# Optimization experiments

Hardware: AMD Instinct MI355X
Metric: run time of the kernel (lower is better)

## Reference

```python
import jax, jax.numpy as jnp
import numpy as np

EMBED = 768
HEADS = 12
HEAD_DIM = EMBED // HEADS  # 64
NUM_CLS = 1
WIN = 16        # one-sided window radius
DIL = 4         # dilation
THETA = 10000.0
COORD_HIGH = 100000.0


def _rotate_half(x):
    # [..., x1, x2, ...] -> [..., -x2, x1, ...] over adjacent pairs
    x1 = x[..., 0::2]
    x2 = x[..., 1::2]
    return jnp.stack([-x2, x1], axis=-1).reshape(x.shape)


def _rope2d(x, coords):
    # x: (B, H, L, head_dim); coords: (B, L, 2) pixel coords
    half = HEAD_DIM // 2
    inv_freq = 1.0 / THETA ** (jnp.arange(0, half, 2, dtype=jnp.float32) / half)  # (half/2,)
    xy = coords.astype(jnp.float32) / COORD_HIGH
    fx = xy[..., 0:1] * inv_freq  # (B, L, half/2)
    fy = xy[..., 1:2] * inv_freq
    fx = jnp.repeat(fx, 2, axis=-1)  # (B, L, half)
    fy = jnp.repeat(fy, 2, axis=-1)
    freqs = jnp.concatenate([fx, fy], axis=-1)  # (B, L, head_dim)
    cos = jnp.cos(freqs)[:, None]  # (B, 1, L, head_dim)
    sin = jnp.sin(freqs)[:, None]
    return x * cos + _rotate_half(x) * sin


def setup_inputs() -> dict:
    key = jax.random.key(0)
    ks = jax.random.split(key, 5)
    B, L = 1, 4096
    S = L + NUM_CLS
    x = jax.random.normal(ks[0], (B, S, EMBED), jnp.float32)
    coords = jax.random.randint(ks[1], (B, L, 2), 0, 100000).astype(jnp.int32)
    qkv_w = jax.random.normal(ks[2], (3 * EMBED, EMBED), jnp.float32) * 0.02
    qkv_b = jnp.zeros((3 * EMBED,), jnp.float32)
    out_w = jax.random.normal(ks[3], (EMBED, EMBED), jnp.float32) * 0.02
    out_b = jnp.zeros((EMBED,), jnp.float32)
    return {"x": x, "coords": coords, "qkv_w": qkv_w, "qkv_b": qkv_b,
            "out_w": out_w, "out_b": out_b}


def reference(x, coords, qkv_w, qkv_b, out_w, out_b):
    B, S, E = x.shape
    L = S - NUM_CLS
    # QKV projection -> (3, B, H, S, hd)
    qkv = (x @ qkv_w.T + qkv_b).reshape(B, S, 3, HEADS, HEAD_DIM)
    qkv = qkv.transpose(2, 0, 3, 1, 4)
    q, k, v = qkv[0], qkv[1], qkv[2]
    # 2D RoPE on patch tokens only
    q = jnp.concatenate([q[:, :, :NUM_CLS], _rope2d(q[:, :, NUM_CLS:], coords)], axis=2)
    k = jnp.concatenate([k[:, :, :NUM_CLS], _rope2d(k[:, :, NUM_CLS:], coords)], axis=2)
    scale = 1.0 / np.sqrt(HEAD_DIM).astype(np.float32)

    q_cls, k_cls, v_cls = q[:, :, :NUM_CLS], k[:, :, :NUM_CLS], v[:, :, :NUM_CLS]
    q_p, k_p, v_p = q[:, :, NUM_CLS:], k[:, :, NUM_CLS:], v[:, :, NUM_CLS:]

    # CLS (global) queries attend to everything
    cls_scores = jnp.einsum('bhqd,bhkd->bhqk', q_cls, k) * scale
    cls_out = jnp.einsum('bhqk,bhkd->bhqd', jax.nn.softmax(cls_scores, axis=-1), v)

    # Patch queries: single softmax over [CLS keys | dilated local window]
    win_len = 2 * WIN + 1
    pos = jnp.arange(L)
    rel = (jnp.arange(win_len) - WIN) * DIL
    key_idx = pos[:, None] + rel[None, :]          # (L, W) absolute patch key index
    valid = (key_idx >= 0) & (key_idx < L)         # boundary patches: masked, not wrapped
    gidx = jnp.clip(key_idx, 0, L - 1)
    k_win = jnp.take(k_p, gidx, axis=2)            # (B, H, L, W, hd)
    v_win = jnp.take(v_p, gidx, axis=2)
    s_win = jnp.einsum('bhld,bhlwd->bhlw', q_p, k_win) * scale
    s_win = jnp.where(valid[None, None], s_win, -jnp.inf)
    s_cls = jnp.einsum('bhld,bhcd->bhlc', q_p, k_cls) * scale
    attn = jax.nn.softmax(jnp.concatenate([s_cls, s_win], axis=-1), axis=-1)
    a_cls, a_win = attn[..., :NUM_CLS], attn[..., NUM_CLS:]
    patch_out = (jnp.einsum('bhlc,bhcd->bhld', a_cls, v_cls)
                 + jnp.einsum('bhlw,bhlwd->bhld', a_win, v_win))

    out = jnp.concatenate([cls_out, patch_out], axis=2)   # (B, H, S, hd)
    out = out.transpose(0, 2, 1, 3).reshape(B, S, E)
    return out @ out_w.T + out_b
```

## Files before the change

### kernel.cpp

```cpp
#include <hip/hip_runtime.h>
#include <hip/hip_bf16.h>

namespace {

constexpr int kS = 4097;
constexpr int kL = 4096;
constexpr int kE = 768;
constexpr int kH = 12;
constexpr int kD = 64;
constexpr int kQKVN = 2304;
constexpr int kT = 1024;
constexpr int kClsChunks = 32;
constexpr int kClsStride = 68;
constexpr float kScale = 0.125f;

typedef short short8 __attribute__((ext_vector_type(8)));
typedef short short4v __attribute__((ext_vector_type(4)));
typedef float f32x4 __attribute__((ext_vector_type(4)));

__device__ inline short f2bf(float x) {
  __hip_bfloat16 b = __float2bfloat16(x);
  return *reinterpret_cast<short*>(&b);
}
__device__ inline float bf2f(short u) {
  unsigned int x = ((unsigned int)(unsigned short)u) << 16;
  union { unsigned int u32; float f; } c;
  c.u32 = x;
  return c.f;
}

__device__ inline void store_c(float* p, float v) { *p = v; }
__device__ inline void store_c(short* p, float v) { *p = f2bf(v); }

#define GLOAD_LDS16(g, l)                                                        \
  __builtin_amdgcn_global_load_lds(                                              \
      (const __attribute__((address_space(1))) unsigned int*)(g),                \
      (__attribute__((address_space(3))) unsigned int*)(l), 16, 0, 0)

__global__ __launch_bounds__(256) void cvt3_kernel(const float* __restrict__ x,
                                                   const float* __restrict__ w,
                                                   const float* __restrict__ ow,
                                                   short* __restrict__ xb,
                                                   short* __restrict__ wb,
                                                   short* __restrict__ owb,
                                                   int n4x, int n4w, int n4o) {
  const int total = n4x + n4w + n4o;
  int i = blockIdx.x * blockDim.x + threadIdx.x;
  const int stride = gridDim.x * blockDim.x;
  for (; i < total; i += stride) {
    const float* src;
    short* dst;
    int k;
    if (i < n4x) { src = x; dst = xb; k = i; }
    else if (i < n4x + n4w) { src = w; dst = wb; k = i - n4x; }
    else { src = ow; dst = owb; k = i - n4x - n4w; }
    f32x4 v = reinterpret_cast<const f32x4*>(src)[k];
    short4v o;
#pragma unroll
    for (int j = 0; j < 4; ++j) o[j] = f2bf(v[j]);
    reinterpret_cast<short4v*>(dst)[k] = o;
  }
}

template <bool ROPE, typename TC>
__global__ __launch_bounds__(256) void gemm_tile_kernel(const short* __restrict__ A,
                                                        const short* __restrict__ W,
                                                        const float* __restrict__ bias,
                                                        TC* __restrict__ C,
                                                        int Mreal, int N, int K,
                                                        const int* __restrict__ coords) {
  __shared__ short Ash[2][128 * 32];
  __shared__ short Bsh[2][128 * 32];
  const int t = threadIdx.x;
  const int lane = t & 63;
  const int wave = t >> 6;
  const int wr = wave >> 1, wc = wave & 1;
  const int m0 = blockIdx.x * 128;
  const int n0 = blockIdx.y * 128;
  const int lrow = lane & 15;
  const int kg = (lane >> 4) << 3;

  const int srow = t >> 2;
  const int scol = (t & 3) << 3;
  int arow0 = m0 + srow;       if (arow0 > Mreal - 1) arow0 = Mreal - 1;
  int arow1 = m0 + 64 + srow;  if (arow1 > Mreal - 1) arow1 = Mreal - 1;
  const int brow0 = n0 + srow;
  const int brow1 = n0 + 64 + srow;

  const size_t aoff0 = (size_t)arow0 * K + scol;
  const size_t aoff1 = (size_t)arow1 * K + scol;
  const size_t boff0 = (size_t)brow0 * K + scol;
  const size_t boff1 = (size_t)brow1 * K + scol;

#define STAGE(buf, k0)                                      \
  do {                                                      \
    GLOAD_LDS16(A + aoff0 + (k0), &Ash[buf][t * 8]);        \
    GLOAD_LDS16(A + aoff1 + (k0), &Ash[buf][2048 + t * 8]); \
    GLOAD_LDS16(W + boff0 + (k0), &Bsh[buf][t * 8]);        \
    GLOAD_LDS16(W + boff1 + (k0), &Bsh[buf][2048 + t * 8]); \
  } while (0)

  f32x4 acc[4][4] = {};

  STAGE(0, 0);
  __syncthreads();

  int cur = 0;
  for (int k0 = 0; k0 < K; k0 += 32) {
    if (k0 + 32 < K) STAGE(cur ^ 1, k0 + 32);

    short8 a[4], b[4];
#pragma unroll
    for (int mi = 0; mi < 4; ++mi)
      a[mi] = *reinterpret_cast<const short8*>(&Ash[cur][(wr * 64 + mi * 16 + lrow) * 32 + kg]);
#pragma unroll
    for (int ni = 0; ni < 4; ++ni)
      b[ni] = *reinterpret_cast<const short8*>(&Bsh[cur][(wc * 64 + ni * 16 + lrow) * 32 + kg]);
#pragma unroll
    for (int mi = 0; mi < 4; ++mi)
#pragma unroll
      for (int ni = 0; ni < 4; ++ni)
        acc[mi][ni] = __builtin_amdgcn_mfma_f32_16x16x32_bf16(a[mi], b[ni], acc[mi][ni], 0, 0, 0);

    __syncthreads();
    cur ^= 1;
  }
#undef STAGE

  const int rg = (lane >> 4) << 2;
  for (int ni = 0; ni < 4; ++ni) {
    const int col = n0 + wc * 64 + ni * 16 + lrow;
    const float bz = bias[col];
    const int sec = col / 768;
    const int dh = col & 63;
    const bool odd = dh & 1;
    const int jf = (dh >> 1) & 15;
    const bool usex = (dh >> 1) < 16;
    const float invf = __powf(10000.0f, -(float)jf * (1.0f / 16.0f));
    for (int mi = 0; mi < 4; ++mi) {
      const int rowb = m0 + wr * 64 + mi * 16 + rg;
#pragma unroll
      for (int r = 0; r < 4; ++r) {
        const int row = rowb + r;
        float v = acc[mi][ni][r] + bz;
        if (ROPE && sec != 2) {
          const float partner = __shfl_xor(v, 1);
          float cs = 1.f, sn = 0.f;
          if (row > 0) {
            const int cl = min(row, kS - 1) - 1;
            const float cx = (float)coords[cl * 2] * 1e-5f;
            const float cy = (float)coords[cl * 2 + 1] * 1e-5f;
            __sincosf((usex ? cx : cy) * invf, &sn, &cs);
          }
          v = odd ? (v * cs + partner * sn) : (v * cs - partner * sn);
          if (sec == 0) v *= kScale;
        }
        if (row < Mreal) store_c(&C[(size_t)row * N + col], v);
      }
    }
  }
}

__global__ __launch_bounds__(256) void attn_kernel(const short* __restrict__ qkv,
                                                   short* __restrict__ attn,
                                                   float* __restrict__ part) {
  __shared__ short Pl[4][32][104];
  __shared__ float sm[4], sl[4], sa[4][64];
  const int lane = threadIdx.x & 63;
  const int wv = threadIdx.x >> 6;

  if (blockIdx.x >= 384) {
    const int idx = blockIdx.x - 384;
    const int h = idx >> 5;
    const int c = idx & 31;
    const int start = c * 128;
    const int end = (c == kClsChunks - 1) ? kS : start + 128;
    const float qd = bf2f(qkv[h * kD + lane]);
    float m = -INFINITY, lsum = 0.f, acc = 0.f;
    for (int s = start + wv; s < end; s += 4) {
      float tt = qd * bf2f(qkv[(size_t)s * kQKVN + kE + h * kD + lane]);
      tt += __shfl_xor(tt, 1); tt += __shfl_xor(tt, 2); tt += __shfl_xor(tt, 4);
      tt += __shfl_xor(tt, 8); tt += __shfl_xor(tt, 16); tt += __shfl_xor(tt, 32);
      const float vd = bf2f(qkv[(size_t)s * kQKVN + 2 * kE + h * kD + lane]);
      const float mnew = fmaxf(m, tt);
      const float cor = __expf(m - mnew);
      const float p = __expf(tt - mnew);
      lsum = lsum * cor + p;
      acc = acc * cor + p * vd;
      m = mnew;
    }
    sa[wv][lane] = acc;
    if (lane == 0) { sm[wv] = m; sl[wv] = lsum; }
    __syncthreads();
    if (wv == 0) {
      float M = fmaxf(fmaxf(sm[0], sm[1]), fmaxf(sm[2], sm[3]));
      float Lt = 0.f, Av = 0.f;
#pragma unroll
      for (int w = 0; w < 4; ++w) {
        const float cw = __expf(sm[w] - M);
        Lt += sl[w] * cw;
        Av += sa[w][lane] * cw;
      }
      float* p = part + ((size_t)h * kClsChunks + c) * kClsStride;
      p[lane] = Av;
      if (lane == 0) { p[64] = M; p[65] = Lt; }
    }
    return;
  }

  const int unit = blockIdx.x * 4 + wv;
  const int t0 = (unit & 31) * 32;
  const int res = (unit >> 5) & 3;
  const int h = unit >> 7;
  const int lrow = lane & 15;
  const int lgrp = lane >> 4;
  const int kg = lgrp * 8;
  const int rg = lgrp * 4;

  f32x4 s_acc[2][4] = {};
  f32x4 s_cls[2] = {};
  short8 aq[2][2];
#pragma unroll
  for (int mi = 0; mi < 2; ++mi) {
    const int tq = t0 + mi * 16 + lrow;
    const size_t row = (size_t)(4 * tq + res + 1) * kQKVN + h * kD;
#pragma unroll
    for (int ks = 0; ks < 2; ++ks)
      aq[mi][ks] = *reinterpret_cast<const short8*>(qkv + row + ks * 32 + kg);
  }
#pragma unroll
  for (int ni = 0; ni < 4; ++ni) {
    int u = t0 - 16 + ni * 16 + lrow;
    u = min(max(u, 0), kT - 1);
    const size_t row = (size_t)(4 * u + res + 1) * kQKVN + kE + h * kD;
    short8 bk[2];
#pragma unroll
    for (int ks = 0; ks < 2; ++ks)
      bk[ks] = *reinterpret_cast<const short8*>(qkv + row + ks * 32 + kg);
#pragma unroll
    for (int mi = 0; mi < 2; ++mi)
#pragma unroll
      for (int ks = 0; ks < 2; ++ks)
        s_acc[mi][ni] = __builtin_amdgcn_mfma_f32_16x16x32_bf16(aq[mi][ks], bk[ks], s_acc[mi][ni], 0, 0, 0);
  }
  {
    short8 bc[2] = {};
    if (lrow == 0) {
#pragma unroll
      for (int ks = 0; ks < 2; ++ks)
        bc[ks] = *reinterpret_cast<const short8*>(qkv + kE + h * kD + ks * 32 + kg);
    }
#pragma unroll
    for (int mi = 0; mi < 2; ++mi)
#pragma unroll
      for (int ks = 0; ks < 2; ++ks)
        s_cls[mi] = __builtin_amdgcn_mfma_f32_16x16x32_bf16(aq[mi][ks], bc[ks], s_cls[mi], 0, 0, 0);
  }

#pragma unroll
  for (int i = 0; i < 2; ++i) {
    const int idx = i * 64 + lane;
    const int q = idx >> 2, ch = idx & 3;
    short8 z = {};
    *reinterpret_cast<short8*>(&Pl[wv][q][64 + ch * 8]) = z;
  }

#pragma unroll
  for (int mi = 0; mi < 2; ++mi) {
#pragma unroll
    for (int r = 0; r < 4; ++r) {
      const int q = mi * 16 + rg + r;
      float sw[4];
      float m = -INFINITY;
#pragma unroll
      for (int ni = 0; ni < 4; ++ni) {
        const int kk = ni * 16 + lrow;
        const int u = t0 - 16 + kk;
        const bool valid = (kk >= q) & (kk <= q + 32) & (u >= 0) & (u < kT);
        sw[ni] = valid ? s_acc[mi][ni][r] : -INFINITY;
        m = fmaxf(m, sw[ni]);
      }
      float scl = (lrow == 0) ? s_cls[mi][r] : -INFINITY;
      m = fmaxf(m, scl);
      m = fmaxf(m, __shfl_xor(m, 1)); m = fmaxf(m, __shfl_xor(m, 2));
      m = fmaxf(m, __shfl_xor(m, 4)); m = fmaxf(m, __shfl_xor(m, 8));
      float lsum = 0.f, ps[4];
#pragma unroll
      for (int ni = 0; ni < 4; ++ni) { ps[ni] = __expf(sw[ni] - m); lsum += ps[ni]; }
      const float pc = __expf(scl - m);
      lsum += pc;
      lsum += __shfl_xor(lsum, 1); lsum += __shfl_xor(lsum, 2);
      lsum += __shfl_xor(lsum, 4); lsum += __shfl_xor(lsum, 8);
      const float inv = __builtin_amdgcn_rcpf(lsum);
#pragma unroll
      for (int ni = 0; ni < 4; ++ni) Pl[wv][q][ni * 16 + lrow] = f2bf(ps[ni] * inv);
      if (lrow == 0) Pl[wv][q][64] = f2bf(pc * inv);
    }
  }

  f32x4 o_acc[4][2] = {};
#pragma unroll
  for (int ks = 0; ks < 3; ++ks) {
    short8 bp[2];
#pragma unroll
    for (int nq = 0; nq < 2; ++nq)
      bp[nq] = *reinterpret_cast<const short8*>(&Pl[wv][nq * 16 + lrow][ks * 32 + kg]);
    short8 av[4];
#pragma unroll
    for (int md = 0; md < 4; ++md) {
      if (ks < 2) {
        const int d = md * 16 + lrow;
#pragma unroll
        for (int e = 0; e < 8; ++e) {
          const int kk = ks * 32 + kg + e;
          int u = t0 - 16 + kk;
          u = min(max(u, 0), kT - 1);
          av[md][e] = qkv[(size_t)(4 * u + res + 1) * kQKVN + 2 * kE + h * kD + d];
        }
      } else {
        short8 z = {};
        av[md] = z;
        if (lgrp == 0)
          av[md][0] = qkv[2 * kE + h * kD + md * 16 + lrow];
      }
#pragma unroll
      for (int nq = 0; nq < 2; ++nq)
        o_acc[md][nq] = __builtin_amdgcn_mfma_f32_16x16x32_bf16(av[md], bp[nq], o_acc[md][nq], 0, 0, 0);
    }
  }

#pragma unroll
  for (int md = 0; md < 4; ++md)
#pragma unroll
    for (int nq = 0; nq < 2; ++nq)
#pragma unroll
      for (int r = 0; r < 4; ++r) {
        const int d = md * 16 + rg + r;
        const int q = nq * 16 + lrow;
        const int s = 4 * (t0 + q) + res + 1;
        attn[(size_t)s * kE + h * kD + d] = f2bf(o_acc[md][nq][r]);
      }
}

__global__ __launch_bounds__(64) void cls_combine_kernel(const float* __restrict__ part,
                                                         short* __restrict__ attn) {
  const int h = blockIdx.x;
  const int lane = threadIdx.x;
  float mc[kClsChunks], lc[kClsChunks], ac[kClsChunks];
#pragma unroll
  for (int c = 0; c < kClsChunks; ++c) {
    const float* p = part + ((size_t)h * kClsChunks + c) * kClsStride;
    mc[c] = p[64];
    lc[c] = p[65];
    ac[c] = p[lane];
  }
  float M = -INFINITY;
#pragma unroll
  for (int c = 0; c < kClsChunks; ++c) M = fmaxf(M, mc[c]);
  float L = 0.f, A = 0.f;
#pragma unroll
  for (int c = 0; c < kClsChunks; ++c) {
    const float w = __expf(mc[c] - M);
    L += lc[c] * w;
    A += ac[c] * w;
  }
  attn[h * kD + lane] = f2bf(A / L);
}

}

extern "C" void kernel_launch(void* const* d_in, const int* in_sizes, int n_in,
                              void* d_out, int out_size, void* d_ws, size_t ws_size,
                              hipStream_t stream) {
  const float* x = (const float*)d_in[0];
  const int* coords = (const int*)d_in[1];
  const float* qkv_w = (const float*)d_in[2];
  const float* qkv_b = (const float*)d_in[3];
  const float* out_w = (const float*)d_in[4];
  const float* out_b = (const float*)d_in[5];
  float* out = (float*)d_out;

  char* p = (char*)d_ws;
  short* qkvb = (short*)p;                p += (size_t)kS * kQKVN * sizeof(short);
  short* xb = (short*)p;                  p += (size_t)kS * kE * sizeof(short);
  short* wb = (short*)p;                  p += (size_t)kQKVN * kE * sizeof(short);
  short* owb = (short*)p;                 p += (size_t)kE * kE * sizeof(short);
  short* attnb = (short*)p;               p += (size_t)kS * kE * sizeof(short);
  float* clsp = (float*)p;

  const int n4x = kS * kE / 4;
  const int n4w = kQKVN * kE / 4;
  const int n4o = kE * kE / 4;
  cvt3_kernel<<<2048, 256, 0, stream>>>(x, qkv_w, out_w, xb, wb, owb, n4x, n4w, n4o);

  dim3 g1(33, 18);
  gemm_tile_kernel<true, short><<<g1, 256, 0, stream>>>(xb, wb, qkv_b, qkvb, kS, kQKVN, kE, coords);
  attn_kernel<<<768, 256, 0, stream>>>(qkvb, attnb, clsp);
  cls_combine_kernel<<<kH, 64, 0, stream>>>(clsp, attnb);
  dim3 g2(33, 6);
  gemm_tile_kernel<false, float><<<g2, 256, 0, stream>>>(attnb, owb, out_b, out, kS, kE, kE, nullptr);
}
```

Baseline: 104.7 us.

## Stage GEMM tiles through registers and swizzle blocks across XCDs

Replaces the direct global-to-LDS async loads with register-staged prefetch: the next K-slice is loaded into registers before the MFMA work, then written to the alternate LDS buffer after a barrier. The grid is flattened to 1D and remapped with an XCD-aware swizzle so that consecutive tiles sharing A or B rows land on the same XCD for L2 reuse. This adds register pressure and an extra barrier per K step in exchange for better load/compute overlap and cache locality.

```diff
diff --git a/kernel.cpp b/kernel.cpp
--- a/kernel.cpp
+++ b/kernel.cpp
@@ -32,10 +32,11 @@
 __device__ inline void store_c(float* p, float v) { *p = v; }
 __device__ inline void store_c(short* p, float v) { *p = f2bf(v); }
 
-#define GLOAD_LDS16(g, l)                                                        \
-  __builtin_amdgcn_global_load_lds(                                              \
-      (const __attribute__((address_space(1))) unsigned int*)(g),                \
-      (__attribute__((address_space(3))) unsigned int*)(l), 16, 0, 0)
+__device__ inline int xcd_swz(int bid, int nwg) {
+  const int q = nwg >> 3, r = nwg & 7;
+  const int x = bid & 7, o = bid >> 3;
+  return (x < r ? x * (q + 1) : r * (q + 1) + (x - r) * q) + o;
+}
 
 __global__ __launch_bounds__(256) void cvt3_kernel(const float* __restrict__ x,
                                                    const float* __restrict__ w,
@@ -67,16 +68,18 @@
                                                         const short* __restrict__ W,
                                                         const float* __restrict__ bias,
                                                         TC* __restrict__ C,
-                                                        int Mreal, int N, int K,
+                                                        int Mreal, int N, int K, int ntm,
                                                         const int* __restrict__ coords) {
   __shared__ short Ash[2][128 * 32];
   __shared__ short Bsh[2][128 * 32];
+  const int nwg = gridDim.x;
+  const int wid = xcd_swz(blockIdx.x, nwg);
+  const int m0 = (wid % ntm) * 128;
+  const int n0 = (wid / ntm) * 128;
   const int t = threadIdx.x;
   const int lane = t & 63;
   const int wave = t >> 6;
   const int wr = wave >> 1, wc = wave & 1;
-  const int m0 = blockIdx.x * 128;
-  const int n0 = blockIdx.y * 128;
   const int lrow = lane & 15;
   const int kg = (lane >> 4) << 3;
 
@@ -87,27 +90,35 @@
   const int brow0 = n0 + srow;
   const int brow1 = n0 + 64 + srow;
 
-  const size_t aoff0 = (size_t)arow0 * K + scol;
-  const size_t aoff1 = (size_t)arow1 * K + scol;
-  const size_t boff0 = (size_t)brow0 * K + scol;
-  const size_t boff1 = (size_t)brow1 * K + scol;
-
-#define STAGE(buf, k0)                                      \
-  do {                                                      \
-    GLOAD_LDS16(A + aoff0 + (k0), &Ash[buf][t * 8]);        \
-    GLOAD_LDS16(A + aoff1 + (k0), &Ash[buf][2048 + t * 8]); \
-    GLOAD_LDS16(W + boff0 + (k0), &Bsh[buf][t * 8]);        \
-    GLOAD_LDS16(W + boff1 + (k0), &Bsh[buf][2048 + t * 8]); \
-  } while (0)
+  const short* pa0 = A + (size_t)arow0 * K + scol;
+  const short* pa1 = A + (size_t)arow1 * K + scol;
+  const short* pb0 = W + (size_t)brow0 * K + scol;
+  const short* pb1 = W + (size_t)brow1 * K + scol;
 
   f32x4 acc[4][4] = {};
-
-  STAGE(0, 0);
-  __syncthreads();
+  const int nsteps = K / 32;
+
+  short8 rA0 = *reinterpret_cast<const short8*>(pa0);
+  short8 rA1 = *reinterpret_cast<const short8*>(pa1);
+  short8 rB0 = *reinterpret_cast<const short8*>(pb0);
+  short8 rB1 = *reinterpret_cast<const short8*>(pb1);
+  *reinterpret_cast<short8*>(&Ash[0][t * 8]) = rA0;
+  *reinterpret_cast<short8*>(&Ash[0][2048 + t * 8]) = rA1;
+  *reinterpret_cast<short8*>(&Bsh[0][t * 8]) = rB0;
+  *reinterpret_cast<short8*>(&Bsh[0][2048 + t * 8]) = rB1;
+  asm volatile("s_waitcnt lgkmcnt(0)" ::: "memory");
+  __builtin_amdgcn_s_barrier();
+  __builtin_amdgcn_sched_barrier(0);
 
   int cur = 0;
-  for (int k0 = 0; k0 < K; k0 += 32) {
-    if (k0 + 32 < K) STAGE(cur ^ 1, k0 + 32);
+  for (int tt = 0; tt < nsteps; ++tt) {
+    if (tt + 1 < nsteps) {
+      const int k1 = (tt + 1) * 32;
+      rA0 = *reinterpret_cast<const short8*>(pa0 + k1);
+      rA1 = *reinterpret_cast<const short8*>(pa1 + k1);
+      rB0 = *reinterpret_cast<const short8*>(pb0 + k1);
+      rB1 = *reinterpret_cast<const short8*>(pb1 + k1);
+    }
 
     short8 a[4], b[4];
 #pragma unroll
@@ -122,10 +133,21 @@
       for (int ni = 0; ni < 4; ++ni)
         acc[mi][ni] = __builtin_amdgcn_mfma_f32_16x16x32_bf16(a[mi], b[ni], acc[mi][ni], 0, 0, 0);
 
-    __syncthreads();
+    __builtin_amdgcn_s_barrier();
+    __builtin_amdgcn_sched_barrier(0);
+
+    if (tt + 1 < nsteps) {
+      *reinterpret_cast<short8*>(&Ash[cur ^ 1][t * 8]) = rA0;
+      *reinterpret_cast<short8*>(&Ash[cur ^ 1][2048 + t * 8]) = rA1;
+      *reinterpret_cast<short8*>(&Bsh[cur ^ 1][t * 8]) = rB0;
+      *reinterpret_cast<short8*>(&Bsh[cur ^ 1][2048 + t * 8]) = rB1;
+    }
+    asm volatile("s_waitcnt lgkmcnt(0)" ::: "memory");
+    __builtin_amdgcn_sched_barrier(0);
+    __builtin_amdgcn_s_barrier();
+    __builtin_amdgcn_sched_barrier(0);
     cur ^= 1;
   }
-#undef STAGE
 
   const int rg = (lane >> 4) << 2;
   for (int ni = 0; ni < 4; ++ni) {
@@ -393,10 +415,8 @@
   const int n4o = kE * kE / 4;
   cvt3_kernel<<<2048, 256, 0, stream>>>(x, qkv_w, out_w, xb, wb, owb, n4x, n4w, n4o);
 
-  dim3 g1(33, 18);
-  gemm_tile_kernel<true, short><<<g1, 256, 0, stream>>>(xb, wb, qkv_b, qkvb, kS, kQKVN, kE, coords);
+  gemm_tile_kernel<true, short><<<594, 256, 0, stream>>>(xb, wb, qkv_b, qkvb, kS, kQKVN, kE, 33, coords);
   attn_kernel<<<768, 256, 0, stream>>>(qkvb, attnb, clsp);
   cls_combine_kernel<<<kH, 64, 0, stream>>>(clsp, attnb);
-  dim3 g2(33, 6);
-  gemm_tile_kernel<false, float><<<g2, 256, 0, stream>>>(attnb, owb, out_b, out, kS, kE, kE, nullptr);
-}
+  gemm_tile_kernel<false, float><<<198, 256, 0, stream>>>(attnb, owb, out_b, out, kS, kE, kE, 33, nullptr);
+}
```

Result: faster. 102.0 us (-2.6%).
